# Kernel tuning notes

Measured on AMD Instinct MI355X. Metric: run time of the kernel, lower is better.

Reference implementation:

```python
import jax, jax.numpy as jnp
import numpy as np

N = 4096        # node_num
D_MODEL = 128   # in_feature == out_feature
QK_DIM = 32
HEAD = 8


def setup_inputs() -> dict:
    key = jax.random.key(0)
    ks = jax.random.split(key, 12)
    s_in = 1.0 / np.sqrt(D_MODEL).astype(np.float32)
    s_hid = 1.0 / np.sqrt(D_MODEL * HEAD).astype(np.float32)
    return {
        "x": jax.random.normal(ks[0], (N, D_MODEL), dtype=jnp.float32),
        "mask": jax.random.randint(ks[1], (N, N), 0, 2) == 1,
        "edge_bias": jax.random.normal(ks[2], (N, N), dtype=jnp.float32),
        # Linear params stored as [in, out] (y = x @ W + b), same math as torch
        "Wq": jax.random.normal(ks[3], (D_MODEL, QK_DIM * HEAD), dtype=jnp.float32) * s_in,
        "bq": jnp.zeros((QK_DIM * HEAD,), dtype=jnp.float32),
        "Wk": jax.random.normal(ks[4], (D_MODEL, QK_DIM * HEAD), dtype=jnp.float32) * s_in,
        "bk": jnp.zeros((QK_DIM * HEAD,), dtype=jnp.float32),
        "Wv": jax.random.normal(ks[5], (D_MODEL, D_MODEL * HEAD), dtype=jnp.float32) * s_in,
        "bv": jnp.zeros((D_MODEL * HEAD,), dtype=jnp.float32),
        "Wo": jax.random.normal(ks[6], (D_MODEL * HEAD, D_MODEL), dtype=jnp.float32) * s_hid,
        "bo": jnp.zeros((D_MODEL,), dtype=jnp.float32),
    }


def reference(x, mask, edge_bias, Wq, bq, Wk, bk, Wv, bv, Wo, bo):
    n = x.shape[0]
    # projections -> [H, N, d]
    q = (x @ Wq + bq).reshape(n, HEAD, QK_DIM).transpose(1, 0, 2)
    k = (x @ Wk + bk).reshape(n, HEAD, QK_DIM).transpose(1, 0, 2)
    v = (x @ Wv + bv).reshape(n, HEAD, D_MODEL).transpose(1, 0, 2)
    inv_sqrt_d = np.float32(1.0 / np.sqrt(QK_DIM))
    scores = jnp.einsum('hnd,hmd->hnm', q, k) * inv_sqrt_d   # [H, N, N]
    scores = scores.at[0].add(edge_bias)                      # edge bias on head 0 only
    scores = jnp.where(mask, jnp.float32(-1e9), scores)      # masked_fill_
    attn = jax.nn.softmax(scores, axis=-1)                    # dropout p=0 (eval)
    res = jnp.einsum('hnm,hmd->hnd', attn, v)                 # [H, N, D_MODEL]
    res = res.transpose(1, 0, 2).reshape(n, D_MODEL * HEAD)
    return res @ Wo + bo                                      # [N, D_MODEL]
```

## Files before the change

### kernel.cpp

```cpp
#include <hip/hip_runtime.h>

#define N_NODES 4096
#define D_MODEL 128
#define QK_DIM  32
#define NHEAD   8
#define QKH     (QK_DIM * NHEAD)
#define VH      (D_MODEL * NHEAD)

typedef _Float16 f16;
typedef _Float16 f16x8 __attribute__((ext_vector_type(8)));
typedef float    f32x4 __attribute__((ext_vector_type(4)));
typedef unsigned long long u64;

static __device__ __forceinline__ unsigned int pack_f16x2(float a, float b) {
    union { f16 h; unsigned short s; } ua, ub;
    ua.h = (f16)a; ub.h = (f16)b;
    return ((unsigned int)ub.s << 16) | (unsigned int)ua.s;
}

__global__ __launch_bounds__(256) void prep_kernel(
    const int* __restrict__ mask, u64* __restrict__ mbits,
    const float* __restrict__ x, f16* __restrict__ xf,
    const float* __restrict__ Wq, const float* __restrict__ Wk,
    f16* __restrict__ Wqkt,
    const float* __restrict__ Wv, f16* __restrict__ Wvt,
    const float* __restrict__ Wo, f16* __restrict__ Wot) {
    const int b = blockIdx.x, t = threadIdx.x;
    if (b < 1024) {
        const int gw = b * 4 + (t >> 6), lane = t & 63;
        for (int word = gw; word < 262144; word += 4096) {
            const int v = mask[(size_t)word * 64 + lane];
            const u64 bits = __ballot(v != 0);
            if (lane == 0) mbits[word] = bits;
        }
    } else if (b < 1280) {
        const int tid = (b - 1024) * 256 + t;
        const float2* x2 = (const float2*)x;
        unsigned int* u = (unsigned int*)xf;
        for (int i = tid; i < 262144; i += 65536) {
            const float2 v = x2[i];
            u[i] = pack_f16x2(v.x, v.y);
        }
    } else if (b < 1408) {
        const int tid = (b - 1280) * 256 + t;
        const int n = tid >> 7, k = tid & 127;
        Wqkt[tid] = (f16)Wq[(size_t)k * QKH + n];
    } else if (b < 1536) {
        const int tid = (b - 1408) * 256 + t;
        const int n = tid >> 7, k = tid & 127;
        Wqkt[32768 + tid] = (f16)Wk[(size_t)k * QKH + n];
    } else if (b < 2048) {
        const int tid = (b - 1536) * 256 + t;
        const int n = tid >> 7, k = tid & 127;
        Wvt[tid] = (f16)Wv[(size_t)k * VH + n];
    } else {
        const int tid = (b - 2048) * 256 + t;
        const int n = tid >> 10, k = tid & 1023;
        Wot[tid] = (f16)Wo[(size_t)k * D_MODEL + n];
    }
}

template <int OUT_MODE, bool DUAL_BIAS>
static __device__ __forceinline__ void gemm_body(
    const f16* __restrict__ A, const f16* __restrict__ Wt,
    const float* __restrict__ b1, const float* __restrict__ b2,
    void* __restrict__ outp, int M, int N, int K,
    int bx, int by, int bz, int nz, void* __restrict__ outp2 = nullptr) {
    const int t = threadIdx.x;
    const int w = t >> 6, lane = t & 63, quad = lane >> 4, col = lane & 15;
    const int mb = by * 64 + (w & 1) * 32;
    const int nb = bx * 64 + (w >> 1) * 32;

    const f32x4 zero = {0.f, 0.f, 0.f, 0.f};
    f32x4 acc[2][2];
    acc[0][0] = zero; acc[0][1] = zero; acc[1][0] = zero; acc[1][1] = zero;

    const int ksteps = K >> 5;
    const int kper = ksteps / nz;
    const int ks0 = bz * kper, ks1 = ks0 + kper;
    for (int ks = ks0; ks < ks1; ++ks) {
        const int ko = ks * 32 + quad * 8;
        const f16x8 a0 = *reinterpret_cast<const f16x8*>(&A[(size_t)(mb + col) * K + ko]);
        const f16x8 a1 = *reinterpret_cast<const f16x8*>(&A[(size_t)(mb + 16 + col) * K + ko]);
        const f16x8 b0 = *reinterpret_cast<const f16x8*>(&Wt[(size_t)(nb + col) * K + ko]);
        const f16x8 bb = *reinterpret_cast<const f16x8*>(&Wt[(size_t)(nb + 16 + col) * K + ko]);
        acc[0][0] = __builtin_amdgcn_mfma_f32_16x16x32_f16(a0, b0, acc[0][0], 0, 0, 0);
        acc[1][0] = __builtin_amdgcn_mfma_f32_16x16x32_f16(a1, b0, acc[1][0], 0, 0, 0);
        acc[0][1] = __builtin_amdgcn_mfma_f32_16x16x32_f16(a0, bb, acc[0][1], 0, 0, 0);
        acc[1][1] = __builtin_amdgcn_mfma_f32_16x16x32_f16(a1, bb, acc[1][1], 0, 0, 0);
    }

    if constexpr (OUT_MODE == 1) {
        __shared__ f16 ct[64][68];
#pragma unroll
        for (int sub = 0; sub < 2; ++sub)
#pragma unroll
            for (int snb = 0; snb < 2; ++snb) {
                const int nl = (w >> 1) * 32 + snb * 16 + col;
                const float bv = b1[nb + snb * 16 + col];
                const int ml0 = (w & 1) * 32 + sub * 16 + quad * 4;
                uint2 u;
                u.x = pack_f16x2(acc[sub][snb][0] + bv, acc[sub][snb][1] + bv);
                u.y = pack_f16x2(acc[sub][snb][2] + bv, acc[sub][snb][3] + bv);
                *reinterpret_cast<uint2*>(&ct[nl][ml0]) = u;
            }
        __syncthreads();
        const int nl = t >> 2, qtr = t & 3;
        const int n = bx * 64 + nl;
        const int m0 = by * 64 + qtr * 16;
        const f16x8 v0 = *reinterpret_cast<const f16x8*>(&ct[nl][qtr * 16]);
        const f16x8 v1 = *reinterpret_cast<const f16x8*>(&ct[nl][qtr * 16 + 8]);
        const int hh = n >> 7, dd = n & 127;
        const int wdv = dd >> 5, t2v = (dd >> 4) & 1, colv = dd & 15;
        {
            const int m = m0;
            const int jb = m >> 6, ksv = (m >> 5) & 1, qv = (m >> 3) & 3;
            const size_t gidx = ((size_t)((((hh * 64 + jb) * 4 + wdv) * 4) + t2v * 2 + ksv)) * 64 + qv * 16 + colv;
            *reinterpret_cast<f16x8*>(&((f16*)outp)[gidx * 8]) = v0;
        }
        {
            const int m = m0 + 8;
            const int jb = m >> 6, ksv = (m >> 5) & 1, qv = (m >> 3) & 3;
            const size_t gidx = ((size_t)((((hh * 64 + jb) * 4 + wdv) * 4) + t2v * 2 + ksv)) * 64 + qv * 16 + colv;
            *reinterpret_cast<f16x8*>(&((f16*)outp)[gidx * 8]) = v1;
        }
    } else if constexpr (OUT_MODE == 4) {
        f16* Qf = (f16*)outp;
        f16* Kf = (f16*)outp2;
#pragma unroll
        for (int sub = 0; sub < 2; ++sub)
#pragma unroll
            for (int snb = 0; snb < 2; ++snb) {
                const int n = nb + snb * 16 + col;
                const float bv = (DUAL_BIAS && n >= 256) ? b2[n - 256] : b1[n];
#pragma unroll
                for (int reg = 0; reg < 4; ++reg) {
                    const int m = mb + sub * 16 + quad * 4 + reg;
                    const float v  = acc[sub][snb][reg] + bv;
                    const float v2 = __shfl_xor(v, 1);
                    if ((lane & 1) == 0) {
                        const int n0 = n & ~1;
                        f16* dst;
                        if (n0 < 256) {
                            dst = &Qf[(size_t)m * 256 + n0];
                        } else {
                            const int d32 = n0 - 256;
                            const int hh = d32 >> 5, dd = d32 & 31;
                            const int lane_k = (dd >> 3) * 16 + ((m >> 2) & 15);
                            const size_t fidx = ((size_t)((hh * 64 + (m >> 6)) * 4 + (m & 3))) * 64 + lane_k;
                            dst = &Kf[fidx * 8 + (dd & 7)];
                        }
                        *reinterpret_cast<unsigned int*>(dst) = pack_f16x2(v, v2);
                    }
                }
            }
    } else {
#pragma unroll
        for (int sub = 0; sub < 2; ++sub)
#pragma unroll
            for (int snb = 0; snb < 2; ++snb) {
                const int n = nb + snb * 16 + col;
                float* ob = (float*)outp + (size_t)bz * M * N;
#pragma unroll
                for (int reg = 0; reg < 4; ++reg) {
                    const int m = mb + sub * 16 + quad * 4 + reg;
                    ob[(size_t)m * N + n] = acc[sub][snb][reg];
                }
            }
    }
}

__global__ __launch_bounds__(256) void proj_kernel(
    const f16* __restrict__ xf, const f16* __restrict__ Wqkt,
    const f16* __restrict__ Wvt,
    const float* __restrict__ bq, const float* __restrict__ bk,
    const float* __restrict__ bv,
    f16* __restrict__ Qf, f16* __restrict__ Kf, f16* __restrict__ Vf) {
    if (blockIdx.x < 8)
        gemm_body<4, true>(xf, Wqkt, bq, bk, Qf, N_NODES, 512, D_MODEL,
                           blockIdx.x, blockIdx.y, 0, 1, Kf);
    else
        gemm_body<1, false>(xf, Wvt, bv, bv, Vf, N_NODES, VH, D_MODEL,
                            blockIdx.x - 8, blockIdx.y, 0, 1);
}

__global__ __launch_bounds__(256) void outproj_kernel(
    const f16* __restrict__ Rf, const f16* __restrict__ Wot,
    float* __restrict__ outp) {
    gemm_body<3, false>(Rf, Wot, nullptr, nullptr, outp, N_NODES, D_MODEL, VH,
                        blockIdx.x, blockIdx.y, blockIdx.z, gridDim.z);
}

#define FENCED_BARRIER() do { \
    asm volatile("s_waitcnt lgkmcnt(0)\n\ts_barrier" ::: "memory"); \
    __builtin_amdgcn_sched_barrier(0); \
} while (0)

#define LOADK(KB, J) do { _Pragma("unroll") \
    for (int km = 0; km < 4; ++km) \
        KB[km] = *reinterpret_cast<const f16x8*>( \
            &Kf[((size_t)((h * 64 + ((J) >> 6)) * 4 + km) * 64 + lane) * 8]); } while (0)

#define LOADV(VB, J) do { _Pragma("unroll") \
    for (int t2 = 0; t2 < 2; ++t2) { _Pragma("unroll") \
        for (int ks = 0; ks < 2; ++ks) \
            VB[t2][ks] = *reinterpret_cast<const f16x8*>( \
                &Vf[((size_t)(((h * 64 + ((J) >> 6)) * 4 + w) * 4 + t2 * 2 + ks) * 64 + lane) * 8]); } } while (0)

#define LOADM(J) do { _Pragma("unroll") \
    for (int reg = 0; reg < 4; ++reg) \
        mr[reg] = mbits[(size_t)(q0 + 16 * w + quad * 4 + reg) * 64 + ((J) >> 6)]; } while (0)

#define LOADB(J) do { _Pragma("unroll") \
    for (int reg = 0; reg < 4; ++reg) { \
        const float4 b4 = *reinterpret_cast<const float4*>( \
            &bias[(size_t)(q0 + 16 * w + quad * 4 + reg) * N_NODES + (J) + 4 * col]); \
        bfr[reg][0] = b4.x; bfr[reg][1] = b4.y; \
        bfr[reg][2] = b4.z; bfr[reg][3] = b4.w; } } while (0)

#define TILE(KB, PSEL, PJ, POK, VJ, MJ, MOK) do { \
    f32x4 S[4]; \
    _Pragma("unroll") \
    for (int km = 0; km < 4; ++km) \
        S[km] = __builtin_amdgcn_mfma_f32_16x16x32_f16(qa, KB[km], zero, 0, 0, 0); \
    if (POK) LOADK(KB, PJ); \
    LOADV(vbT, VJ); \
    _Pragma("unroll") \
    for (int reg = 0; reg < 4; ++reg) { \
        float pk[4]; \
        _Pragma("unroll") \
        for (int km = 0; km < 4; ++km) { \
            float base = C8; \
            if (h == 0) base = __builtin_fmaf(bfr[reg][km], L2E, C8); \
            const float tt = __builtin_fmaf(S[km][reg], SCL, base); \
            const bool msk = (mr[reg] >> (4 * col + km)) & 1ull; \
            pk[km] = msk ? 0.f : __builtin_amdgcn_exp2f(tt); \
        } \
        uint2 u; \
        u.x = pack_f16x2(pk[0], pk[1]); \
        u.y = pack_f16x2(pk[2], pk[3]); \
        *reinterpret_cast<uint2*>(&ps[PSEL][16 * w + quad * 4 + reg][4 * col]) = u; \
    } \
    if (MOK) { LOADM(MJ); if (h == 0) LOADB(MJ); } \
    FENCED_BARRIER(); \
    __builtin_amdgcn_s_setprio(1); \
    _Pragma("unroll") \
    for (int ks = 0; ks < 2; ++ks) { _Pragma("unroll") \
        for (int qs = 0; qs < 4; ++qs) { \
            const f16x8 pa = *reinterpret_cast<const f16x8*>( \
                &ps[PSEL][16 * qs + col][ks * 32 + quad * 8]); \
            if (qs == w) \
                Lacc = __builtin_amdgcn_mfma_f32_16x16x32_f16(pa, onesv, Lacc, 0, 0, 0); \
            O[qs][0] = __builtin_amdgcn_mfma_f32_16x16x32_f16(pa, vbT[0][ks], O[qs][0], 0, 0, 0); \
            O[qs][1] = __builtin_amdgcn_mfma_f32_16x16x32_f16(pa, vbT[1][ks], O[qs][1], 0, 0, 0); \
        } } \
    __builtin_amdgcn_s_setprio(0); \
} while (0)

__global__ __launch_bounds__(256, 3) void attn_kernel(
    const f16* __restrict__ Qf, const f16* __restrict__ Kf,
    const f16* __restrict__ Vf,
    const u64* __restrict__ mbits, const float* __restrict__ bias,
    f16* __restrict__ R, f16* __restrict__ part, float* __restrict__ lsum) {
    const int h  = blockIdx.y;
    const int q0 = blockIdx.x * 64;
    const int t  = threadIdx.x;
    const int w = t >> 6, lane = t & 63, quad = lane >> 4, col = lane & 15;

    __shared__ f16 ps[2][64][72];
    __shared__ float ls[64];

    const f16x8 qa = *reinterpret_cast<const f16x8*>(
        &Qf[(size_t)(q0 + 16 * w + col) * 256 + h * 32 + quad * 8]);

    const f32x4 zero = {0.f, 0.f, 0.f, 0.f};
    f32x4 O[4][2];
#pragma unroll
    for (int qs = 0; qs < 4; ++qs) { O[qs][0] = zero; O[qs][1] = zero; }
    f32x4 Lacc = zero;
    const f16 one1 = (f16)1.f;
    const f16x8 onesv = {one1, one1, one1, one1, one1, one1, one1, one1};

    const float L2E = 1.4426950408889634f;
    const float SCL = 0.17677669529663687f * 1.4426950408889634f;
    const float C8  = -8.f * 1.4426950408889634f;
    const int jspan = N_NODES / gridDim.z;
    const int jbegin = blockIdx.z * jspan, jend = jbegin + jspan;

    f16x8 kbA[4], kbB[4];
    f16x8 vbT[2][2];
    u64   mr[4];
    float bfr[4][4];

    LOADK(kbA, jbegin);
    LOADK(kbB, jbegin + 64);
    LOADM(jbegin);
    if (h == 0) LOADB(jbegin);

    for (int j0 = jbegin; j0 < jend; j0 += 128) {
        TILE(kbA, 0, j0 + 128, j0 + 128 < jend, j0,      j0 + 64,  true);
        TILE(kbB, 1, j0 + 192, j0 + 192 < jend, j0 + 64, j0 + 128, j0 + 128 < jend);
    }

    if (col == 0) {
#pragma unroll
        for (int reg = 0; reg < 4; ++reg)
            ls[16 * w + quad * 4 + reg] = Lacc[reg];
    }
    __syncthreads();

    if (gridDim.z == 1) {
#pragma unroll
        for (int qs = 0; qs < 4; ++qs)
#pragma unroll
            for (int reg = 0; reg < 4; ++reg) {
                const float inv = 1.f / ls[16 * qs + quad * 4 + reg];
                const int q = q0 + 16 * qs + quad * 4 + reg;
#pragma unroll
                for (int t2 = 0; t2 < 2; ++t2)
                    R[(size_t)q * VH + h * 128 + 32 * w + 16 * t2 + col] =
                        (f16)(O[qs][t2][reg] * inv);
            }
    } else {
        const size_t seg = (size_t)(blockIdx.z * NHEAD + h) * N_NODES;
#pragma unroll
        for (int qs = 0; qs < 4; ++qs)
#pragma unroll
            for (int reg = 0; reg < 4; ++reg) {
                const float inv = 1.f / ls[16 * qs + quad * 4 + reg];
                const int q = q0 + 16 * qs + quad * 4 + reg;
#pragma unroll
                for (int t2 = 0; t2 < 2; ++t2)
                    part[(seg + q) * 128 + 32 * w + 16 * t2 + col] =
                        (f16)(O[qs][t2][reg] * inv);
            }
        if (col == 0) {
#pragma unroll
            for (int reg = 0; reg < 4; ++reg)
                lsum[seg + q0 + 16 * w + quad * 4 + reg] = Lacc[reg];
        }
    }
}

__global__ __launch_bounds__(256) void merge_kernel(
    const f16* __restrict__ part, const float* __restrict__ lsum,
    f16* __restrict__ R, int split) {
    const int tid = blockIdx.x * 256 + threadIdx.x;
    const int d8 = tid & 15, q = (tid >> 4) & 4095, h = tid >> 16;
    float acc[8];
#pragma unroll
    for (int i = 0; i < 8; ++i) acc[i] = 0.f;
    float den = 0.f;
    for (int z = 0; z < split; ++z) {
        const size_t seg = (size_t)(z * NHEAD + h) * N_NODES + q;
        const float l = lsum[seg];
        const f16x8 v = *reinterpret_cast<const f16x8*>(&part[seg * 128 + 8 * d8]);
#pragma unroll
        for (int i = 0; i < 8; ++i) acc[i] += l * (float)v[i];
        den += l;
    }
    const float inv = 1.f / den;
    f16x8 o;
#pragma unroll
    for (int i = 0; i < 8; ++i) o[i] = (f16)(acc[i] * inv);
    *reinterpret_cast<f16x8*>(&R[(size_t)q * VH + h * 128 + 8 * d8]) = o;
}

__global__ __launch_bounds__(256) void reduce_out_kernel(
    const float* __restrict__ part, const float* __restrict__ bo,
    float* __restrict__ out) {
    const int i = (blockIdx.x * 256 + threadIdx.x) * 4;
    float4 s = *reinterpret_cast<const float4*>(&bo[i & 127]);
#pragma unroll
    for (int z = 0; z < 4; ++z) {
        const float4 p = *reinterpret_cast<const float4*>(
            &part[(size_t)z * N_NODES * D_MODEL + i]);
        s.x += p.x; s.y += p.y; s.z += p.z; s.w += p.w;
    }
    *reinterpret_cast<float4*>(&out[i]) = s;
}

extern "C" void kernel_launch(void* const* d_in, const int* in_sizes, int n_in,
                              void* d_out, int out_size, void* d_ws, size_t ws_size,
                              hipStream_t stream) {
    const float* x  = (const float*)d_in[0];
    const int*   mk = (const int*)d_in[1];
    const float* eb = (const float*)d_in[2];
    const float* Wq = (const float*)d_in[3];
    const float* bq = (const float*)d_in[4];
    const float* Wk = (const float*)d_in[5];
    const float* bk = (const float*)d_in[6];
    const float* Wv = (const float*)d_in[7];
    const float* bv = (const float*)d_in[8];
    const float* Wo = (const float*)d_in[9];
    const float* bo = (const float*)d_in[10];
    float* out = (float*)d_out;

    char* ws = (char*)d_ws;
    u64* mbits = (u64*)(ws);
    f16* xf16 = (f16*)(ws + 2097152);
    f16* Wqkt = (f16*)(ws + 3145728);
    f16* Wvt  = (f16*)(ws + 3276800);
    f16* Wot  = (f16*)(ws + 3538944);
    f16* Qf   = (f16*)(ws + 3801088);
    f16* Kf   = (f16*)(ws + 5898240);
    f16* Vf   = (f16*)(ws + 7995392);
    f16* Rf   = (f16*)(ws + 16384000);
    float* out_part = (float*)(ws + 24772608);
    float* lsum = (float*)(ws + 33161216);
    f16* part = (f16*)(ws + 33685504);

    int split = 1;
    if (ws_size >= 67239936ull) split = 4;
    else if (ws_size >= 50462720ull) split = 2;
    const bool ksplit_out = ws_size >= 33161216ull;

    prep_kernel<<<2560, 256, 0, stream>>>(mk, mbits, x, xf16, Wq, Wk, Wqkt, Wv, Wvt, Wo, Wot);

    proj_kernel<<<dim3(24, 64), 256, 0, stream>>>(xf16, Wqkt, Wvt, bq, bk, bv, Qf, Kf, Vf);

    attn_kernel<<<dim3(64, 8, split), 256, 0, stream>>>(Qf, Kf, Vf, mbits, eb, Rf, part, lsum);
    if (split > 1)
        merge_kernel<<<2048, 256, 0, stream>>>(part, lsum, Rf, split);

    if (ksplit_out) {
        outproj_kernel<<<dim3(2, 64, 4), 256, 0, stream>>>(Rf, Wot, out_part);
        reduce_out_kernel<<<512, 256, 0, stream>>>(out_part, bo, out);
    } else {
        outproj_kernel<<<dim3(2, 64, 1), 256, 0, stream>>>(Rf, Wot, out_part);
        reduce_out_kernel<<<512, 256, 0, stream>>>(out_part, bo, out);
    }
}
```

Baseline: 299.2 us.

## Pre-swizzle GEMM operands into MFMA fragment order for coalesced loads

Operands for the projection and output GEMMs (x, Wqk, Wv, Wo, and the attention result R) are now stored in a blocked layout where each 16-row by 32-k MFMA fragment is contiguous. Each lane then reads its f16x8 from consecutive addresses instead of strided rows. The prep kernel is rewritten to emit this layout with 8-wide vector stores and needs fewer blocks. In exchange, the weight transposes in prep read strided and the attention and merge writes to R become scattered.

```diff
diff --git a/kernel.cpp b/kernel.cpp
--- a/kernel.cpp
+++ b/kernel.cpp
@@ -34,29 +34,54 @@
             if (lane == 0) mbits[word] = bits;
         }
     } else if (b < 1280) {
-        const int tid = (b - 1024) * 256 + t;
-        const float2* x2 = (const float2*)x;
-        unsigned int* u = (unsigned int*)xf;
-        for (int i = tid; i < 262144; i += 65536) {
-            const float2 v = x2[i];
-            u[i] = pack_f16x2(v.x, v.y);
+        const int c = (b - 1024) * 256 + t;
+        const int fidx = c >> 6, lanep = c & 63;
+        const int rblk = fidx >> 2, ks = fidx & 3;
+        const int row = rblk * 16 + (lanep & 15);
+        const int kb = ks * 32 + (lanep >> 4) * 8;
+        const float4 f0 = *reinterpret_cast<const float4*>(&x[(size_t)row * 128 + kb]);
+        const float4 f1 = *reinterpret_cast<const float4*>(&x[(size_t)row * 128 + kb + 4]);
+        f16x8 o;
+        o[0] = (f16)f0.x; o[1] = (f16)f0.y; o[2] = (f16)f0.z; o[3] = (f16)f0.w;
+        o[4] = (f16)f1.x; o[5] = (f16)f1.y; o[6] = (f16)f1.z; o[7] = (f16)f1.w;
+        *reinterpret_cast<f16x8*>(&xf[(size_t)c * 8]) = o;
+    } else if (b < 1312) {
+        const int c = (b - 1280) * 256 + t;
+        const int fidx = c >> 6, lanep = c & 63;
+        const int nblk = fidx >> 2, ks = fidx & 3;
+        const int n = nblk * 16 + (lanep & 15);
+        const int kb = ks * 32 + (lanep >> 4) * 8;
+        f16x8 o;
+#pragma unroll
+        for (int e = 0; e < 8; ++e) {
+            const int k = kb + e;
+            const float v = (n < 256) ? Wq[(size_t)k * 256 + n]
+                                      : Wk[(size_t)k * 256 + (n - 256)];
+            o[e] = (f16)v;
         }
-    } else if (b < 1408) {
-        const int tid = (b - 1280) * 256 + t;
-        const int n = tid >> 7, k = tid & 127;
-        Wqkt[tid] = (f16)Wq[(size_t)k * QKH + n];
-    } else if (b < 1536) {
-        const int tid = (b - 1408) * 256 + t;
-        const int n = tid >> 7, k = tid & 127;
-        Wqkt[32768 + tid] = (f16)Wk[(size_t)k * QKH + n];
-    } else if (b < 2048) {
-        const int tid = (b - 1536) * 256 + t;
-        const int n = tid >> 7, k = tid & 127;
-        Wvt[tid] = (f16)Wv[(size_t)k * VH + n];
-    } else {
-        const int tid = (b - 2048) * 256 + t;
-        const int n = tid >> 10, k = tid & 1023;
-        Wot[tid] = (f16)Wo[(size_t)k * D_MODEL + n];
+        *reinterpret_cast<f16x8*>(&Wqkt[(size_t)c * 8]) = o;
+    } else if (b < 1376) {
+        const int c = (b - 1312) * 256 + t;
+        const int fidx = c >> 6, lanep = c & 63;
+        const int nblk = fidx >> 2, ks = fidx & 3;
+        const int n = nblk * 16 + (lanep & 15);
+        const int kb = ks * 32 + (lanep >> 4) * 8;
+        f16x8 o;
+#pragma unroll
+        for (int e = 0; e < 8; ++e)
+            o[e] = (f16)Wv[(size_t)(kb + e) * 1024 + n];
+        *reinterpret_cast<f16x8*>(&Wvt[(size_t)c * 8]) = o;
+    } else if (b < 1440) {
+        const int c = (b - 1376) * 256 + t;
+        const int fidx = c >> 6, lanep = c & 63;
+        const int nblk = fidx >> 5, ks = fidx & 31;
+        const int n = nblk * 16 + (lanep & 15);
+        const int kb = ks * 32 + (lanep >> 4) * 8;
+        f16x8 o;
+#pragma unroll
+        for (int e = 0; e < 8; ++e)
+            o[e] = (f16)Wo[(size_t)(kb + e) * 128 + n];
+        *reinterpret_cast<f16x8*>(&Wot[(size_t)c * 8]) = o;
     }
 }
 
@@ -78,12 +103,16 @@
     const int ksteps = K >> 5;
     const int kper = ksteps / nz;
     const int ks0 = bz * kper, ks1 = ks0 + kper;
+    const int rblk0 = mb >> 4, nblk0 = nb >> 4;
     for (int ks = ks0; ks < ks1; ++ks) {
-        const int ko = ks * 32 + quad * 8;
-        const f16x8 a0 = *reinterpret_cast<const f16x8*>(&A[(size_t)(mb + col) * K + ko]);
-        const f16x8 a1 = *reinterpret_cast<const f16x8*>(&A[(size_t)(mb + 16 + col) * K + ko]);
-        const f16x8 b0 = *reinterpret_cast<const f16x8*>(&Wt[(size_t)(nb + col) * K + ko]);
-        const f16x8 bb = *reinterpret_cast<const f16x8*>(&Wt[(size_t)(nb + 16 + col) * K + ko]);
+        const f16x8 a0 = *reinterpret_cast<const f16x8*>(
+            &A[((size_t)(rblk0 * ksteps + ks) * 64 + lane) * 8]);
+        const f16x8 a1 = *reinterpret_cast<const f16x8*>(
+            &A[((size_t)((rblk0 + 1) * ksteps + ks) * 64 + lane) * 8]);
+        const f16x8 b0 = *reinterpret_cast<const f16x8*>(
+            &Wt[((size_t)(nblk0 * ksteps + ks) * 64 + lane) * 8]);
+        const f16x8 bb = *reinterpret_cast<const f16x8*>(
+            &Wt[((size_t)((nblk0 + 1) * ksteps + ks) * 64 + lane) * 8]);
         acc[0][0] = __builtin_amdgcn_mfma_f32_16x16x32_f16(a0, b0, acc[0][0], 0, 0, 0);
         acc[1][0] = __builtin_amdgcn_mfma_f32_16x16x32_f16(a1, b0, acc[1][0], 0, 0, 0);
         acc[0][1] = __builtin_amdgcn_mfma_f32_16x16x32_f16(a0, bb, acc[0][1], 0, 0, 0);
@@ -317,9 +346,12 @@
                 const float inv = 1.f / ls[16 * qs + quad * 4 + reg];
                 const int q = q0 + 16 * qs + quad * 4 + reg;
 #pragma unroll
-                for (int t2 = 0; t2 < 2; ++t2)
-                    R[(size_t)q * VH + h * 128 + 32 * w + 16 * t2 + col] =
-                        (f16)(O[qs][t2][reg] * inv);
+                for (int t2 = 0; t2 < 2; ++t2) {
+                    const int hd = h * 128 + 32 * w + 16 * t2 + col;
+                    const size_t c = ((size_t)(q >> 4) * 32 + (hd >> 5)) * 64 +
+                                     ((hd >> 3) & 3) * 16 + (q & 15);
+                    R[c * 8 + (hd & 7)] = (f16)(O[qs][t2][reg] * inv);
+                }
             }
     } else {
         const size_t seg = (size_t)(blockIdx.z * NHEAD + h) * N_NODES;
@@ -363,7 +395,9 @@
     f16x8 o;
 #pragma unroll
     for (int i = 0; i < 8; ++i) o[i] = (f16)(acc[i] * inv);
-    *reinterpret_cast<f16x8*>(&R[(size_t)q * VH + h * 128 + 8 * d8]) = o;
+    const size_t c = ((size_t)(q >> 4) * 32 + h * 4 + (d8 >> 2)) * 64 +
+                     (d8 & 3) * 16 + (q & 15);
+    *reinterpret_cast<f16x8*>(&R[c * 8]) = o;
 }
 
 __global__ __launch_bounds__(256) void reduce_out_kernel(
@@ -415,7 +449,7 @@
     else if (ws_size >= 50462720ull) split = 2;
     const bool ksplit_out = ws_size >= 33161216ull;
 
-    prep_kernel<<<2560, 256, 0, stream>>>(mk, mbits, x, xf16, Wq, Wk, Wqkt, Wv, Wvt, Wo, Wot);
+    prep_kernel<<<1440, 256, 0, stream>>>(mk, mbits, x, xf16, Wq, Wk, Wqkt, Wv, Wvt, Wo, Wot);
 
     proj_kernel<<<dim3(24, 64), 256, 0, stream>>>(xf16, Wqkt, Wvt, bq, bk, bv, Qf, Kf, Vf);
 
```

Result: no change. 300.7 us (+0.5%).
